# Kernel tuning notes

Measured on AMD Instinct MI355X. Metric: run time of the kernel, lower is better.

## Reference

```python
import jax, jax.numpy as jnp
import numpy as np

V = 25  # joints

def _normalize_adjacency_chain(adjacency: np.ndarray) -> np.ndarray:
    A = adjacency.astype(np.float32).copy()
    A += np.eye(A.shape[0], dtype=np.float32)
    row_sum = A.sum(axis=1, keepdims=True)
    row_sum[row_sum == 0.0] = 1.0
    return A / row_sum


def setup_inputs() -> dict:
    key = jax.random.key(0)
    k_x, k_w, k_b = jax.random.split(key, 3)
    N, C_in, C_out, T = 32, 256, 256, 300
    x = jax.random.normal(k_x, (N, C_in, V, T), dtype=jnp.float32)
    # chain adjacency over V joints, normalized with self-loops (module buffer)
    adj = np.zeros((V, V), dtype=np.float32)
    for i in range(V - 1):
        adj[i, i + 1] = 1.0
        adj[i + 1, i] = 1.0
    A = jnp.asarray(_normalize_adjacency_chain(adj))
    # 1x1 Conv2d params: weight (C_out, C_in), bias (C_out,)
    fan_in = C_in  # kernel 1x1
    bound = 1.0 / np.sqrt(fan_in)
    W = jax.random.uniform(k_w, (C_out, C_in), minval=-bound, maxval=bound, dtype=jnp.float32)
    b = jax.random.uniform(k_b, (C_out,), minval=-bound, maxval=bound, dtype=jnp.float32)
    return {"x": x, "A": A, "W": W, "b": b}


def reference(x, A, W, b):
    # x: (N, C, V, T); A: (V, V) row-normalized adjacency with self-loops
    agg = jnp.einsum('ncvt,vw->ncwt', x, A)          # graph aggregation
    out = jnp.einsum('ncvt,oc->novt', agg, W)        # 1x1 conv = channel GEMM
    return out + b[None, :, None, None]
```

## Files before the change

kernel.cpp:

```cpp
#include <hip/hip_runtime.h>

typedef unsigned short u16;
typedef unsigned int u32;
typedef __attribute__((ext_vector_type(8))) short short8;
typedef __attribute__((ext_vector_type(4))) float f32x4;
typedef __attribute__((ext_vector_type(2))) unsigned int u32x2;
typedef __attribute__((ext_vector_type(4))) unsigned int u32x4;

#define C_IN 256
#define C_OUT 256
#define VJ 25
#define TT 300
#define VT 7500
#define ROWBLKS 59
#define PERN_ELEMS (ROWBLKS * 4 * 128 * 64)
#define WB_ELEMS (256 * 256)
#define NTOT 32

__device__ __forceinline__ u16 f2bf(float f) {
  u32 u = __float_as_uint(f);
  u32 r = (u + 0x7fffu + ((u >> 16) & 1u)) >> 16;
  return (u16)r;
}

__global__ void k0_wcast(const float* __restrict__ W, u16* __restrict__ Wb) {
  int i = (blockIdx.x * 256 + threadIdx.x) * 4;
  f32x4 w = *(const f32x4*)(W + i);
  u32x2 pk;
  pk[0] = (u32)f2bf(w[0]) | ((u32)f2bf(w[1]) << 16);
  pk[1] = (u32)f2bf(w[2]) | ((u32)f2bf(w[3]) << 16);
  *(u32x2*)(Wb + i) = pk;
}

__global__ __launch_bounds__(256, 2) void k_pipe(
    const float* __restrict__ x, const float* __restrict__ A,
    const u16* __restrict__ Wb, const float* __restrict__ bias,
    float* __restrict__ out, u16* __restrict__ aggT,
    int k1_base, int k2_base, int nslots) {
  __shared__ __attribute__((aligned(16))) unsigned char smem[58016];
  const int tid = threadIdx.x;
  const int bx = blockIdx.x;
  const int zz = blockIdx.z;

  if (bx < 76) {
    const int n = k1_base + zz;
    if (n >= NTOT) return;
    u16* agg_s = (u16*)smem;
    float(*cw)[4] = (float(*)[4])(smem + 57600);
    const int tblk = bx % 19;
    const int cblk = bx / 19;

    if (tid < 25) {
      int w = tid;
      cw[w][0] = (w > 0) ? A[(w - 1) * 25 + w] : 0.0f;
      cw[w][1] = A[w * 25 + w];
      cw[w][2] = (w < 24) ? A[(w + 1) * 25 + w] : 0.0f;
    }
    __syncthreads();

    const int tq = tid & 3;
    const int c = tid >> 2;
    const int t0 = tblk * 16 + tq * 4;
    const int tb = (t0 <= TT - 4) ? t0 : (TT - 4);
    const int cg = cblk * 64 + c;

    const float* xp = x + ((size_t)n * C_IN + cg) * VT + tb;
    f32x4 xv[25];
#pragma unroll
    for (int v = 0; v < 25; ++v) xv[v] = *(const f32x4*)(xp + v * TT);

#pragma unroll
    for (int w = 0; w < 25; ++w) {
      const int wm = (w > 0) ? w - 1 : 0;
      const int wp = (w < 24) ? w + 1 : 24;
      float a0 = cw[w][0], a1 = cw[w][1], a2 = cw[w][2];
#pragma unroll
      for (int i = 0; i < 4; ++i) {
        float r = xv[wm][i] * a0 + xv[w][i] * a1 + xv[wp][i] * a2;
        agg_s[(w * 16 + tq * 4 + i) * 72 + c] = f2bf(r);
      }
    }
    __syncthreads();

    const int c8 = tid & 7;
    const int rb = tid >> 3;
    u16* dstn = aggT + (size_t)(n % nslots) * PERN_ELEMS;
#pragma unroll
    for (int it = 0; it < 13; ++it) {
      int rr = it * 32 + rb;
      if (rr < 400) {
        int w = rr >> 4, ti = rr & 15;
        int t = tblk * 16 + ti;
        if (t < TT) {
          int g = w * TT + t;
          int rowblk = g >> 7, row_in = g & 127;
          u32x4 v = *(const u32x4*)&agg_s[(w * 16 + ti) * 72 + c8 * 8];
          *(u32x4*)(dstn + ((size_t)(rowblk * 4 + cblk) * 128 + row_in) * 64 + c8 * 8) = v;
        }
      }
    }
  } else {
    const int n = k2_base + zz;
    if (n < 0 || n >= NTOT) return;
    u16* As = (u16*)smem;
    u16* Bs = (u16*)(smem + 16384);
    const int bxx = bx - 76;
    const int cb = bxx % 59;
    const int ob = bxx / 59;
    const int l = tid & 63;
    const int wv = tid >> 6;
    const int wm = wv & 1, wn = wv >> 1;
    const int m = l & 15, quad = l >> 4;
    f32x4 acc[4][4] = {};

    const u16* aggn = aggT + (size_t)(n % nslots) * PERN_ELEMS + (size_t)cb * 4 * 8192;
    const u16* wbase = Wb + ob * 128 * 256;

    for (int kb = 0; kb < 4; ++kb) {
#pragma unroll
      for (int i = 0; i < 4; ++i) {
        int ch = i * 256 + tid;
        int row = ch >> 3, jp = ch & 7;
        int jd = jp ^ (row & 7);
        const u16* ga = wbase + row * 256 + kb * 64 + jd * 8;
        __builtin_amdgcn_global_load_lds((const __attribute__((address_space(1))) void*)ga,
                                         (__attribute__((address_space(3))) void*)&As[ch * 8],
                                         16, 0, 0);
        const u16* gb = aggn + kb * 8192 + row * 64 + jd * 8;
        __builtin_amdgcn_global_load_lds((const __attribute__((address_space(1))) void*)gb,
                                         (__attribute__((address_space(3))) void*)&Bs[ch * 8],
                                         16, 0, 0);
      }
      __syncthreads();
#pragma unroll
      for (int ks = 0; ks < 2; ++ks) {
        short8 af[4], bfr[4];
        int jj = ks * 4 + quad;
#pragma unroll
        for (int mi = 0; mi < 4; ++mi) {
          int row = wm * 64 + mi * 16 + m;
          af[mi] = *(const short8*)&As[row * 64 + ((jj ^ (row & 7)) * 8)];
        }
#pragma unroll
        for (int ni = 0; ni < 4; ++ni) {
          int row = wn * 64 + ni * 16 + m;
          bfr[ni] = *(const short8*)&Bs[row * 64 + ((jj ^ (row & 7)) * 8)];
        }
#pragma unroll
        for (int mi = 0; mi < 4; ++mi)
#pragma unroll
          for (int ni = 0; ni < 4; ++ni)
            acc[mi][ni] = __builtin_amdgcn_mfma_f32_16x16x32_bf16(af[mi], bfr[ni], acc[mi][ni], 0, 0, 0);
      }
      __syncthreads();
    }

    float* outn = out + (size_t)n * C_OUT * VT;
    const int colbase = cb * 128 + wn * 64 + m;
#pragma unroll
    for (int mi = 0; mi < 4; ++mi) {
      const int o0 = ob * 128 + wm * 64 + mi * 16 + quad * 4;
      float b0 = bias[o0], b1 = bias[o0 + 1], b2 = bias[o0 + 2], b3 = bias[o0 + 3];
#pragma unroll
      for (int ni = 0; ni < 4; ++ni) {
        int col = colbase + ni * 16;
        if (col < VT) {
          float* p = outn + (size_t)o0 * VT + col;
          p[0]      = acc[mi][ni][0] + b0;
          p[VT]     = acc[mi][ni][1] + b1;
          p[2 * VT] = acc[mi][ni][2] + b2;
          p[3 * VT] = acc[mi][ni][3] + b3;
        }
      }
    }
  }
}

extern "C" void kernel_launch(void* const* d_in, const int* in_sizes, int n_in,
                              void* d_out, int out_size, void* d_ws, size_t ws_size,
                              hipStream_t stream) {
  (void)in_sizes; (void)n_in; (void)out_size;
  const float* x = (const float*)d_in[0];
  const float* A = (const float*)d_in[1];
  const float* W = (const float*)d_in[2];
  const float* bvec = (const float*)d_in[3];
  float* out = (float*)d_out;
  u16* wb = (u16*)d_ws;
  u16* aggT = wb + WB_ELEMS;

  const size_t pern_bytes = (size_t)PERN_ELEMS * 2;
  const size_t base_bytes = (size_t)WB_ELEMS * 2;
  int S = 1;
  if (ws_size > base_bytes + pern_bytes) {
    size_t a = (ws_size - base_bytes) / pern_bytes;
    S = (a >= NTOT) ? NTOT : (int)a;
  }

  k0_wcast<<<64, 256, 0, stream>>>(W, wb);

  if (S >= 2) {
    int b = S / 2;
    if (b > 4) b = 4;
    for (int p = 0; (p - 1) * b < NTOT; ++p) {
      k_pipe<<<dim3(194, 1, b), 256, 0, stream>>>(x, A, wb, bvec, out, aggT,
                                                  p * b, (p - 1) * b, S);
    }
  } else {
    for (int nn = 0; nn < NTOT; ++nn) {
      k_pipe<<<dim3(76, 1, 1), 256, 0, stream>>>(x, A, wb, bvec, out, aggT, nn, -NTOT, 1);
      k_pipe<<<dim3(194, 1, 1), 256, 0, stream>>>(x, A, wb, bvec, out, aggT, NTOT, nn, 1);
    }
  }
}
```

Baseline: 553.3 us.

## Split fused pipeline kernel into stencil and GEMM kernels over large batch chunks

Replaces the single pipelined kernel, which mixed stencil blocks for batch p with GEMM blocks for batch p-1 in small groups, with two separate kernels. Each is launched over as many batches as the workspace holds, often all 32, so there are far fewer launches. The GEMM also gains double-buffered LDS staging, so the load of the next K slice overlaps the MFMA work on the current one. The cost is that stencil and GEMM no longer overlap in time, and with large chunks the intermediate buffer may spill out of cache before the GEMM reads it.

```diff
diff --git a/kernel.cpp b/kernel.cpp
--- a/kernel.cpp
+++ b/kernel.cpp
@@ -32,145 +32,151 @@
   *(u32x2*)(Wb + i) = pk;
 }
 
-__global__ __launch_bounds__(256, 2) void k_pipe(
+__global__ __launch_bounds__(256) void k1_stencil(
     const float* __restrict__ x, const float* __restrict__ A,
-    const u16* __restrict__ Wb, const float* __restrict__ bias,
-    float* __restrict__ out, u16* __restrict__ aggT,
-    int k1_base, int k2_base, int nslots) {
-  __shared__ __attribute__((aligned(16))) unsigned char smem[58016];
+    u16* __restrict__ aggT, int n0) {
+  __shared__ float cw[25][4];
+  __shared__ u16 agg_s[25 * 16 * 72];
   const int tid = threadIdx.x;
-  const int bx = blockIdx.x;
-  const int zz = blockIdx.z;
-
-  if (bx < 76) {
-    const int n = k1_base + zz;
-    if (n >= NTOT) return;
-    u16* agg_s = (u16*)smem;
-    float(*cw)[4] = (float(*)[4])(smem + 57600);
-    const int tblk = bx % 19;
-    const int cblk = bx / 19;
-
-    if (tid < 25) {
-      int w = tid;
-      cw[w][0] = (w > 0) ? A[(w - 1) * 25 + w] : 0.0f;
-      cw[w][1] = A[w * 25 + w];
-      cw[w][2] = (w < 24) ? A[(w + 1) * 25 + w] : 0.0f;
+  const int tblk = blockIdx.x;
+  const int cblk = blockIdx.y;
+  const int nn = blockIdx.z;
+  const int n = n0 + nn;
+
+  if (tid < 25) {
+    int w = tid;
+    cw[w][0] = (w > 0) ? A[(w - 1) * 25 + w] : 0.0f;
+    cw[w][1] = A[w * 25 + w];
+    cw[w][2] = (w < 24) ? A[(w + 1) * 25 + w] : 0.0f;
+  }
+  __syncthreads();
+
+  const int tq = tid & 3;
+  const int c = tid >> 2;
+  const int t0 = tblk * 16 + tq * 4;
+  const int tb = (t0 <= TT - 4) ? t0 : (TT - 4);
+  const int cg = cblk * 64 + c;
+
+  const float* xp = x + ((size_t)n * C_IN + cg) * VT + tb;
+  f32x4 xv[25];
+#pragma unroll
+  for (int v = 0; v < 25; ++v) xv[v] = *(const f32x4*)(xp + v * TT);
+
+#pragma unroll
+  for (int w = 0; w < 25; ++w) {
+    const int wm = (w > 0) ? w - 1 : 0;
+    const int wp = (w < 24) ? w + 1 : 24;
+    float a0 = cw[w][0], a1 = cw[w][1], a2 = cw[w][2];
+#pragma unroll
+    for (int i = 0; i < 4; ++i) {
+      float r = xv[wm][i] * a0 + xv[w][i] * a1 + xv[wp][i] * a2;
+      agg_s[(w * 16 + tq * 4 + i) * 72 + c] = f2bf(r);
+    }
+  }
+  __syncthreads();
+
+  const int c8 = tid & 7;
+  const int rb = tid >> 3;
+  u16* dstn = aggT + (size_t)nn * PERN_ELEMS;
+#pragma unroll
+  for (int it = 0; it < 13; ++it) {
+    int rr = it * 32 + rb;
+    if (rr < 400) {
+      int w = rr >> 4, ti = rr & 15;
+      int t = tblk * 16 + ti;
+      if (t < TT) {
+        int g = w * TT + t;
+        int rowblk = g >> 7, row_in = g & 127;
+        u32x4 v = *(const u32x4*)&agg_s[(w * 16 + ti) * 72 + c8 * 8];
+        *(u32x4*)(dstn + ((size_t)(rowblk * 4 + cblk) * 128 + row_in) * 64 + c8 * 8) = v;
+      }
+    }
+  }
+}
+
+__global__ __launch_bounds__(256, 2) void k2_gemm(
+    const u16* __restrict__ aggT, const u16* __restrict__ Wb,
+    const float* __restrict__ bias, float* __restrict__ out, int n0) {
+  __shared__ u16 As[2][128 * 64];
+  __shared__ u16 Bs[2][128 * 64];
+  const int tid = threadIdx.x;
+  const int cb = blockIdx.x;
+  const int ob = blockIdx.y;
+  const int nn = blockIdx.z;
+  const int n = n0 + nn;
+  const int l = tid & 63;
+  const int wv = tid >> 6;
+  const int wm = wv & 1, wn = wv >> 1;
+  const int m = l & 15, quad = l >> 4;
+  f32x4 acc[4][4] = {};
+
+  const u16* aggn = aggT + (size_t)nn * PERN_ELEMS + (size_t)cb * 4 * 8192;
+  const u16* wbase = Wb + ob * 128 * 256;
+
+  const int ch0 = tid;
+#define STAGE_KB(kb, pb)                                                        \
+  {                                                                             \
+    _Pragma("unroll")                                                           \
+    for (int i = 0; i < 4; ++i) {                                               \
+      int ch = i * 256 + ch0;                                                   \
+      int row = ch >> 3, jp = ch & 7;                                           \
+      int jd = jp ^ (row & 7);                                                  \
+      const u16* ga = wbase + row * 256 + (kb) * 64 + jd * 8;                   \
+      __builtin_amdgcn_global_load_lds(                                         \
+          (const __attribute__((address_space(1))) void*)ga,                    \
+          (__attribute__((address_space(3))) void*)&As[pb][ch * 8], 16, 0, 0);  \
+      const u16* gb = aggn + (kb) * 8192 + row * 64 + jd * 8;                   \
+      __builtin_amdgcn_global_load_lds(                                         \
+          (const __attribute__((address_space(1))) void*)gb,                    \
+          (__attribute__((address_space(3))) void*)&Bs[pb][ch * 8], 16, 0, 0);  \
+    }                                                                           \
+  }
+
+  STAGE_KB(0, 0);
+  __syncthreads();
+
+  for (int kb = 0; kb < 4; ++kb) {
+    const int cur = kb & 1;
+    if (kb < 3) STAGE_KB(kb + 1, cur ^ 1);
+#pragma unroll
+    for (int ks = 0; ks < 2; ++ks) {
+      short8 af[4], bfr[4];
+      int jj = ks * 4 + quad;
+#pragma unroll
+      for (int mi = 0; mi < 4; ++mi) {
+        int row = wm * 64 + mi * 16 + m;
+        af[mi] = *(const short8*)&As[cur][row * 64 + ((jj ^ (row & 7)) * 8)];
+      }
+#pragma unroll
+      for (int ni = 0; ni < 4; ++ni) {
+        int row = wn * 64 + ni * 16 + m;
+        bfr[ni] = *(const short8*)&Bs[cur][row * 64 + ((jj ^ (row & 7)) * 8)];
+      }
+#pragma unroll
+      for (int mi = 0; mi < 4; ++mi)
+#pragma unroll
+        for (int ni = 0; ni < 4; ++ni)
+          acc[mi][ni] = __builtin_amdgcn_mfma_f32_16x16x32_bf16(af[mi], bfr[ni], acc[mi][ni], 0, 0, 0);
     }
     __syncthreads();
-
-    const int tq = tid & 3;
-    const int c = tid >> 2;
-    const int t0 = tblk * 16 + tq * 4;
-    const int tb = (t0 <= TT - 4) ? t0 : (TT - 4);
-    const int cg = cblk * 64 + c;
-
-    const float* xp = x + ((size_t)n * C_IN + cg) * VT + tb;
-    f32x4 xv[25];
-#pragma unroll
-    for (int v = 0; v < 25; ++v) xv[v] = *(const f32x4*)(xp + v * TT);
-
-#pragma unroll
-    for (int w = 0; w < 25; ++w) {
-      const int wm = (w > 0) ? w - 1 : 0;
-      const int wp = (w < 24) ? w + 1 : 24;
-      float a0 = cw[w][0], a1 = cw[w][1], a2 = cw[w][2];
-#pragma unroll
-      for (int i = 0; i < 4; ++i) {
-        float r = xv[wm][i] * a0 + xv[w][i] * a1 + xv[wp][i] * a2;
-        agg_s[(w * 16 + tq * 4 + i) * 72 + c] = f2bf(r);
-      }
-    }
-    __syncthreads();
-
-    const int c8 = tid & 7;
-    const int rb = tid >> 3;
-    u16* dstn = aggT + (size_t)(n % nslots) * PERN_ELEMS;
-#pragma unroll
-    for (int it = 0; it < 13; ++it) {
-      int rr = it * 32 + rb;
-      if (rr < 400) {
-        int w = rr >> 4, ti = rr & 15;
-        int t = tblk * 16 + ti;
-        if (t < TT) {
-          int g = w * TT + t;
-          int rowblk = g >> 7, row_in = g & 127;
-          u32x4 v = *(const u32x4*)&agg_s[(w * 16 + ti) * 72 + c8 * 8];
-          *(u32x4*)(dstn + ((size_t)(rowblk * 4 + cblk) * 128 + row_in) * 64 + c8 * 8) = v;
-        }
-      }
-    }
-  } else {
-    const int n = k2_base + zz;
-    if (n < 0 || n >= NTOT) return;
-    u16* As = (u16*)smem;
-    u16* Bs = (u16*)(smem + 16384);
-    const int bxx = bx - 76;
-    const int cb = bxx % 59;
-    const int ob = bxx / 59;
-    const int l = tid & 63;
-    const int wv = tid >> 6;
-    const int wm = wv & 1, wn = wv >> 1;
-    const int m = l & 15, quad = l >> 4;
-    f32x4 acc[4][4] = {};
-
-    const u16* aggn = aggT + (size_t)(n % nslots) * PERN_ELEMS + (size_t)cb * 4 * 8192;
-    const u16* wbase = Wb + ob * 128 * 256;
-
-    for (int kb = 0; kb < 4; ++kb) {
-#pragma unroll
-      for (int i = 0; i < 4; ++i) {
-        int ch = i * 256 + tid;
-        int row = ch >> 3, jp = ch & 7;
-        int jd = jp ^ (row & 7);
-        const u16* ga = wbase + row * 256 + kb * 64 + jd * 8;
-        __builtin_amdgcn_global_load_lds((const __attribute__((address_space(1))) void*)ga,
-                                         (__attribute__((address_space(3))) void*)&As[ch * 8],
-                                         16, 0, 0);
-        const u16* gb = aggn + kb * 8192 + row * 64 + jd * 8;
-        __builtin_amdgcn_global_load_lds((const __attribute__((address_space(1))) void*)gb,
-                                         (__attribute__((address_space(3))) void*)&Bs[ch * 8],
-                                         16, 0, 0);
-      }
-      __syncthreads();
-#pragma unroll
-      for (int ks = 0; ks < 2; ++ks) {
-        short8 af[4], bfr[4];
-        int jj = ks * 4 + quad;
-#pragma unroll
-        for (int mi = 0; mi < 4; ++mi) {
-          int row = wm * 64 + mi * 16 + m;
-          af[mi] = *(const short8*)&As[row * 64 + ((jj ^ (row & 7)) * 8)];
-        }
-#pragma unroll
-        for (int ni = 0; ni < 4; ++ni) {
-          int row = wn * 64 + ni * 16 + m;
-          bfr[ni] = *(const short8*)&Bs[row * 64 + ((jj ^ (row & 7)) * 8)];
-        }
-#pragma unroll
-        for (int mi = 0; mi < 4; ++mi)
-#pragma unroll
-          for (int ni = 0; ni < 4; ++ni)
-            acc[mi][ni] = __builtin_amdgcn_mfma_f32_16x16x32_bf16(af[mi], bfr[ni], acc[mi][ni], 0, 0, 0);
-      }
-      __syncthreads();
-    }
-
-    float* outn = out + (size_t)n * C_OUT * VT;
-    const int colbase = cb * 128 + wn * 64 + m;
-#pragma unroll
-    for (int mi = 0; mi < 4; ++mi) {
-      const int o0 = ob * 128 + wm * 64 + mi * 16 + quad * 4;
-      float b0 = bias[o0], b1 = bias[o0 + 1], b2 = bias[o0 + 2], b3 = bias[o0 + 3];
-#pragma unroll
-      for (int ni = 0; ni < 4; ++ni) {
-        int col = colbase + ni * 16;
-        if (col < VT) {
-          float* p = outn + (size_t)o0 * VT + col;
-          p[0]      = acc[mi][ni][0] + b0;
-          p[VT]     = acc[mi][ni][1] + b1;
-          p[2 * VT] = acc[mi][ni][2] + b2;
-          p[3 * VT] = acc[mi][ni][3] + b3;
-        }
+  }
+#undef STAGE_KB
+
+  float* outn = out + (size_t)n * C_OUT * VT;
+  const int colbase = cb * 128 + wn * 64 + m;
+#pragma unroll
+  for (int mi = 0; mi < 4; ++mi) {
+    const int o0 = ob * 128 + wm * 64 + mi * 16 + quad * 4;
+    float b0 = bias[o0], b1 = bias[o0 + 1], b2 = bias[o0 + 2], b3 = bias[o0 + 3];
+#pragma unroll
+    for (int ni = 0; ni < 4; ++ni) {
+      int col = colbase + ni * 16;
+      if (col < VT) {
+        float* p = outn + (size_t)o0 * VT + col;
+        p[0]      = acc[mi][ni][0] + b0;
+        p[VT]     = acc[mi][ni][1] + b1;
+        p[2 * VT] = acc[mi][ni][2] + b2;
+        p[3 * VT] = acc[mi][ni][3] + b3;
       }
     }
   }
@@ -183,32 +189,23 @@
   const float* x = (const float*)d_in[0];
   const float* A = (const float*)d_in[1];
   const float* W = (const float*)d_in[2];
-  const float* bvec = (const float*)d_in[3];
+  const float* b = (const float*)d_in[3];
   float* out = (float*)d_out;
   u16* wb = (u16*)d_ws;
   u16* aggT = wb + WB_ELEMS;
 
   const size_t pern_bytes = (size_t)PERN_ELEMS * 2;
   const size_t base_bytes = (size_t)WB_ELEMS * 2;
-  int S = 1;
+  int nchunk = 1;
   if (ws_size > base_bytes + pern_bytes) {
     size_t a = (ws_size - base_bytes) / pern_bytes;
-    S = (a >= NTOT) ? NTOT : (int)a;
+    nchunk = (a >= NTOT) ? NTOT : (int)a;
   }
 
   k0_wcast<<<64, 256, 0, stream>>>(W, wb);
-
-  if (S >= 2) {
-    int b = S / 2;
-    if (b > 4) b = 4;
-    for (int p = 0; (p - 1) * b < NTOT; ++p) {
-      k_pipe<<<dim3(194, 1, b), 256, 0, stream>>>(x, A, wb, bvec, out, aggT,
-                                                  p * b, (p - 1) * b, S);
-    }
-  } else {
-    for (int nn = 0; nn < NTOT; ++nn) {
-      k_pipe<<<dim3(76, 1, 1), 256, 0, stream>>>(x, A, wb, bvec, out, aggT, nn, -NTOT, 1);
-      k_pipe<<<dim3(194, 1, 1), 256, 0, stream>>>(x, A, wb, bvec, out, aggT, NTOT, nn, 1);
-    }
-  }
-}
+  for (int n0 = 0; n0 < NTOT; n0 += nchunk) {
+    int nc = NTOT - n0; if (nc > nchunk) nc = nchunk;
+    k1_stencil<<<dim3(19, 4, nc), 256, 0, stream>>>(x, A, aggT, n0);
+    k2_gemm<<<dim3(59, 2, nc), 256, 0, stream>>>(aggT, wb, b, out, n0);
+  }
+}
```

Result: faster. 529.3 us (-4.3%).
